# Kernel tuning notes

Measured on AMD Instinct MI355X. Metric: run time of the kernel, lower is better.

Reference implementation:

```python
import jax, jax.numpy as jnp
import numpy as np
from jax import lax

H = 512          # hidden_size
STATE = 16       # state_size
K = 4            # conv_kernel
EXPAND = 2
INNER = H * EXPAND
RATIO = 0.5      # remaining_ratio
EPS = 1e-5       # LayerNorm eps (torch default)


def linear(x, w, b=None):
    # torch nn.Linear: y = x @ W^T + b, W stored (out, in)
    y = jnp.einsum('...i,oi->...o', x, w)
    return y + b if b is not None else y


def causal_dwconv(x, w, b):
    # x: (B,S,C); w: (C,1,K) depthwise. torch pads K-1 both sides then slices
    # [:, :, :S], which equals left-pad K-1 (causal).
    xc = jnp.swapaxes(x, 1, 2)  # (B,C,S)
    y = lax.conv_general_dilated(xc, w, (1,), [(K - 1, 0)],
                                 feature_group_count=w.shape[0],
                                 dimension_numbers=('NCH', 'OIH', 'NCH'))
    return jnp.swapaxes(y + b[None, :, None], 1, 2)


def conv1d_same(x, w, b):
    # x: (B,S,C); w: (Cout,Cin,3), padding=1
    xc = jnp.swapaxes(x, 1, 2)
    y = lax.conv_general_dilated(xc, w, (1,), [(1, 1)],
                                 dimension_numbers=('NCH', 'OIH', 'NCH'))
    return jnp.swapaxes(y + b[None, :, None], 1, 2)


def layernorm(x, g, b):
    m = jnp.mean(x, axis=-1, keepdims=True)
    v = jnp.mean((x - m) ** 2, axis=-1, keepdims=True)
    return (x - m) * lax.rsqrt(v + EPS) * g + b


def partial_flip(x):
    S = x.shape[1]
    r = max(1, int(S * RATIO))
    n = S - r
    if n <= 0:
        return x
    return jnp.concatenate([x[:, :n][:, ::-1], x[:, n:]], axis=1)


def mamba_block(x, in_w, conv_w, conv_b, xproj_w, dt_w, dt_b, D, out_w):
    # x: (B,S,H)
    xz = linear(x, in_w)                              # (B,S,2*INNER)
    x_proj, z = xz[..., :INNER], xz[..., INNER:]
    x_conv = jax.nn.silu(causal_dwconv(x_proj, conv_w, conv_b))  # (B,S,INNER)
    xs = linear(x_conv, xproj_w)                      # (B,S,2*STATE+INNER)
    Bm = xs[..., :STATE]
    Cm = xs[..., STATE:2 * STATE]
    dt = jax.nn.softplus(linear(xs[..., 2 * STATE:], dt_w, dt_b))
    # EMA-approx SSM scan
    alpha = jax.nn.sigmoid(dt * 0.1)
    alpha_c = jnp.clip(alpha, 0.01, 0.99)
    B_gate = jax.nn.sigmoid(jnp.mean(Bm, axis=-1, keepdims=True))
    gated = (1.0 - alpha) * B_gate * x_conv

    def step(h, ab):
        a, gi = ab
        h = a * h + gi
        return h, h

    h0 = jnp.zeros((x.shape[0], INNER), x.dtype)
    _, ys = lax.scan(step, h0, (jnp.swapaxes(alpha_c, 0, 1), jnp.swapaxes(gated, 0, 1)))
    y = jnp.swapaxes(ys, 0, 1)                        # (B,S,INNER)
    y = y * jax.nn.sigmoid(jnp.mean(Cm, axis=-1, keepdims=True))
    y = y + D * x_conv
    y = y * jax.nn.silu(z)
    return linear(y, out_w)


def setup_inputs() -> dict:
    key = jax.random.key(0)
    ks = iter(jax.random.split(key, 48))

    def nrm(shape, s=0.02):
        return jax.random.normal(next(ks), shape, jnp.float32) * s

    def dt_bias():
        u = jax.random.uniform(next(ks), (INNER,), jnp.float32)
        return jnp.exp(u * (np.log(0.1) - np.log(0.001)) + np.log(0.001))

    Bsz, S = 4, 4096
    inp = {
        'x': jax.random.normal(next(ks), (Bsz, S, H), jnp.float32),
        'seq_len': jnp.full((Bsz,), S, jnp.int32),
        'ds_w': nrm((H, H)), 'ds_b': jnp.zeros((H,), jnp.float32),
        'gate_w': nrm((H, 2 * H)), 'gate_b': jnp.zeros((H,), jnp.float32),
        'mix_w': nrm((H, H)), 'mix_b': jnp.zeros((H,), jnp.float32),
        'ln_g': jnp.ones((H,), jnp.float32), 'ln_b': jnp.zeros((H,), jnp.float32),
        'fe_c1_w': nrm((H, H, 3)), 'fe_c1_b': jnp.zeros((H,), jnp.float32),
        'fe_c2_w': nrm((H, H, 3)), 'fe_c2_b': jnp.zeros((H,), jnp.float32),
        'fe_ln_g': jnp.ones((H,), jnp.float32), 'fe_ln_b': jnp.zeros((H,), jnp.float32),
    }
    for p in ('f', 'b'):
        inp[p + '_in_w'] = nrm((2 * INNER, H))
        inp[p + '_conv_w'] = nrm((INNER, 1, K))
        inp[p + '_conv_b'] = jnp.zeros((INNER,), jnp.float32)
        inp[p + '_xproj_w'] = nrm((2 * STATE + INNER, INNER))
        inp[p + '_dt_w'] = nrm((INNER, INNER))
        inp[p + '_dt_b'] = dt_bias()
        inp[p + '_D'] = jnp.ones((INNER,), jnp.float32)
        inp[p + '_out_w'] = nrm((H, INNER))
    return inp


def reference(x, seq_len, ds_w, ds_b, gate_w, gate_b, mix_w, mix_b, ln_g, ln_b,
              fe_c1_w, fe_c1_b, fe_c2_w, fe_c2_b, fe_ln_g, fe_ln_b,
              f_in_w, f_conv_w, f_conv_b, f_xproj_w, f_dt_w, f_dt_b, f_D, f_out_w,
              b_in_w, b_conv_w, b_conv_b, b_xproj_w, b_dt_w, b_dt_b, b_D, b_out_w):
    gate_weights = jax.nn.sigmoid(linear(x, ds_w, ds_b))
    m_fwd = mamba_block(x, f_in_w, f_conv_w, f_conv_b, f_xproj_w, f_dt_w, f_dt_b, f_D, f_out_w)
    m_bwd = partial_flip(mamba_block(partial_flip(x), b_in_w, b_conv_w, b_conv_b,
                                     b_xproj_w, b_dt_w, b_dt_b, b_D, b_out_w))
    m_comb = gate_weights * m_fwd + (1.0 - gate_weights) * m_bwd
    # FE conv branch
    c = jax.nn.silu(conv1d_same(x, fe_c1_w, fe_c1_b))
    c = conv1d_same(c, fe_c2_w, fe_c2_b)
    f_out = layernorm(c + x, fe_ln_g, fe_ln_b)
    g = jax.nn.sigmoid(linear(jnp.concatenate([m_comb, f_out], axis=-1), gate_w, gate_b))
    z = g * m_comb + (1.0 - g) * f_out
    z = linear(z, mix_w, mix_b)
    z = layernorm(z + x, ln_g, ln_b)
    return z
```

## Files before the change

kernel.cpp:

```cpp
#include <hip/hip_runtime.h>
#include <math.h>

#define Tt 16384
#define Ss 4096
#define Bb 4
#define Hh 512
#define II 1024
#define CHUNK 32
#define NCH 128
#define SP 4098

typedef unsigned short ushort_t;
typedef unsigned int uint_t;
typedef __attribute__((ext_vector_type(8))) short bf16x8;
typedef __attribute__((ext_vector_type(4))) short bf16x4;
typedef __attribute__((ext_vector_type(4))) float f32x4;

__device__ __forceinline__ float sigm(float x) { return 1.0f / (1.0f + __expf(-x)); }
__device__ __forceinline__ float b2f(ushort_t h) { return __uint_as_float(((uint_t)h) << 16); }
__device__ __forceinline__ ushort_t f2b(float f) {
    uint_t u = __float_as_uint(f);
    return (ushort_t)((u + 0x7FFFu + ((u >> 16) & 1u)) >> 16);
}
__device__ __forceinline__ void stc(float* p, float v)    { *p = v; }
__device__ __forceinline__ void stc(ushort_t* p, float v) { *p = f2b(v); }
__device__ __forceinline__ float ldc1(const float* p)    { return *p; }
__device__ __forceinline__ float ldc1(const ushort_t* p) { return b2f(*p); }

__device__ __forceinline__ void gload16(const void* g, void* l) {
    __builtin_amdgcn_global_load_lds(
        (const __attribute__((address_space(1))) unsigned int*)g,
        (__attribute__((address_space(3))) unsigned int*)l,
        16, 0, 0);
}

__global__ __launch_bounds__(256) void mfma_gemm(
    const ushort_t* __restrict__ A, const ushort_t* __restrict__ A1, int lda,
    const ushort_t* __restrict__ W, int ldw,
    const float* __restrict__ bias,
    void* __restrict__ Cv, int ldc, int Nreal, int K,
    int amode, int act, int smode, int cbf16)
{
    __shared__ __align__(16) ushort_t As[128 * 32];
    __shared__ __align__(16) ushort_t Bs[128 * 32];
    const int tid  = threadIdx.x;
    const int lane = tid & 63;
    const int wid  = tid >> 6;
    const int bm   = blockIdx.y * 128;
    const int bn   = blockIdx.x * 128;
    const int wr   = wid >> 1;
    const int wc   = wid & 1;

    const int colA = (lane & 3) * 8;
    long gA[2], gW[2];
    #pragma unroll
    for (int r = 0; r < 2; ++r) {
        const int rt = (r * 4 + wid) * 16 + (lane >> 2);
        const int t  = bm + rt;
        const int b  = t >> 12;
        const int s  = t & (Ss - 1);
        long rowoff;
        if (amode == 0)      rowoff = (long)t * lda;
        else if (amode == 1) { const int sf = (s < 2048) ? (2047 - s) : s;
                               rowoff = (long)(b * SP + sf + 1) * 512; }
        else if (amode == 2) rowoff = (long)(b * SP + s + 1) * 512;
        else if (amode == 3) rowoff = (long)(b * SP + s) * 512;
        else                 rowoff = (long)t * 512;
        gA[r] = rowoff + colA;
        gW[r] = (long)(bn + rt) * ldw + colA;
    }

    const int aoff = (wr * 64 + (lane & 15)) * 32 + (lane >> 4) * 8;
    const int boff = (wc * 64 + (lane & 15)) * 32 + (lane >> 4) * 8;

    f32x4 acc[4][4] = {};

    for (int k0 = 0; k0 < K; k0 += 32) {
        const ushort_t* pA = A;
        long kadd = k0;
        if (amode == 4) { pA = (k0 < 512) ? A : A1; kadd = k0 & 511; }
        #pragma unroll
        for (int r = 0; r < 2; ++r) {
            gload16(pA + gA[r] + kadd, &As[(r * 4 + wid) * 512]);
            gload16(W + gW[r] + k0,    &Bs[(r * 4 + wid) * 512]);
        }
        __syncthreads();

        bf16x8 af[4], bfr[4];
        #pragma unroll
        for (int mi = 0; mi < 4; ++mi) af[mi]  = *(const bf16x8*)&As[aoff + mi * 512];
        #pragma unroll
        for (int ni = 0; ni < 4; ++ni) bfr[ni] = *(const bf16x8*)&Bs[boff + ni * 512];
        #pragma unroll
        for (int mi = 0; mi < 4; ++mi)
            #pragma unroll
            for (int ni = 0; ni < 4; ++ni)
                acc[mi][ni] = __builtin_amdgcn_mfma_f32_16x16x32_bf16(
                    af[mi], bfr[ni], acc[mi][ni], 0, 0, 0);
        __syncthreads();
    }

    float* Cf = (float*)Cv;
    ushort_t* Cb = (ushort_t*)Cv;
    #pragma unroll
    for (int mi = 0; mi < 4; ++mi) {
        const int row0 = bm + wr * 64 + mi * 16 + (lane >> 4) * 4;
        #pragma unroll
        for (int ni = 0; ni < 4; ++ni) {
            const int col = bn + wc * 64 + ni * 16 + (lane & 15);
            if (col < Nreal) {
                const float bv = bias ? bias[col] : 0.f;
                #pragma unroll
                for (int r = 0; r < 4; ++r) {
                    float v = acc[mi][ni][r] + bv;
                    if (act == 1) v = sigm(v);
                    else if (act == 2) v = v * sigm(v);
                    const int t = row0 + r;
                    long crow;
                    if (smode == 1) { const int b = t >> 12, s = t & (Ss - 1);
                                      crow = (long)(b * SP + s + 1); }
                    else crow = t;
                    if (cbf16) Cb[crow * ldc + col] = f2b(v);
                    else       Cf[crow * ldc + col] = v;
                }
            }
        }
    }
}


__global__ __launch_bounds__(256) void cvt_x_pad(
    const float* __restrict__ x, ushort_t* __restrict__ xpad)
{
    const int idx = blockIdx.x * 256 + threadIdx.x;
    const int c8 = (idx & 63) * 8;
    const int sp = (idx >> 6) % SP;
    const int b  = idx / (64 * SP);
    bf16x8 v;
    if (sp == 0 || sp == SP - 1) {
        v = (bf16x8)0;
    } else {
        const float* p = x + ((long)(b * Ss + sp - 1)) * 512 + c8;
        #pragma unroll
        for (int j = 0; j < 8; ++j) v[j] = (short)f2b(p[j]);
    }
    *(bf16x8*)&xpad[((long)(b * SP + sp)) * 512 + c8] = v;
}

__global__ __launch_bounds__(256) void cvt_plain(
    const float* __restrict__ s, ushort_t* __restrict__ d, int n4)
{
    const int i = blockIdx.x * 256 + threadIdx.x;
    if (i >= n4) return;
    const float4 f = *(const float4*)&s[(long)i * 4];
    bf16x4 v;
    v[0] = (short)f2b(f.x); v[1] = (short)f2b(f.y);
    v[2] = (short)f2b(f.z); v[3] = (short)f2b(f.w);
    *(bf16x4*)&d[(long)i * 4] = v;
}

__global__ __launch_bounds__(256) void cvt_xproj(
    const float* __restrict__ s, ushort_t* __restrict__ d)
{
    const int i = blockIdx.x * 256 + threadIdx.x;
    const long e = (long)i * 4;
    const int n = (int)(e >> 10);
    bf16x4 v = (bf16x4)0;
    if (n < 1056) {
        const float4 f = *(const float4*)&s[e];
        v[0] = (short)f2b(f.x); v[1] = (short)f2b(f.y);
        v[2] = (short)f2b(f.z); v[3] = (short)f2b(f.w);
    }
    *(bf16x4*)&d[e] = v;
}

__global__ __launch_bounds__(256) void cvt_fe(
    const float* __restrict__ s, ushort_t* __restrict__ d)
{
    const int idx = blockIdx.x * 256 + threadIdx.x;
    const int n = idx / 1536;
    const int rem = idx - n * 1536;
    const int j = rem >> 9;
    const int c = rem & 511;
    d[idx] = f2b(s[((long)n * 512 + c) * 3 + j]);
}

__global__ __launch_bounds__(256) void zero_halo(ushort_t* __restrict__ p)
{
    const int i = blockIdx.x * 256 + threadIdx.x;
    const int c8 = (i & 63) * 8;
    const int h = (i >> 6) & 1;
    const int b = i >> 7;
    const long row = (long)b * SP + (h ? SP - 1 : 0);
    *(bf16x8*)&p[row * 512 + c8] = (bf16x8)0;
}


__global__ __launch_bounds__(256) void dwconv_silu_k(
    const ushort_t* __restrict__ xz, const float* __restrict__ w,
    const float* __restrict__ bias, ushort_t* __restrict__ out)
{
    const int idx = blockIdx.x * 256 + threadIdx.x;
    const int c = idx & (II - 1);
    const int t = idx >> 10;
    const int s = t & (Ss - 1);
    const long rb = (long)t * 2048;
    const float w0 = w[c * 4 + 0], w1 = w[c * 4 + 1], w2 = w[c * 4 + 2], w3 = w[c * 4 + 3];
    float sum = bias[c] + b2f(xz[rb + c]) * w3;
    if (s >= 1) sum += b2f(xz[rb - 2048 + c]) * w2;
    if (s >= 2) sum += b2f(xz[rb - 2 * 2048 + c]) * w1;
    if (s >= 3) sum += b2f(xz[rb - 3 * 2048 + c]) * w0;
    out[idx] = f2b(sum * sigm(sum));
}

__global__ __launch_bounds__(256) void bgcg_k(
    const ushort_t* __restrict__ xs, float* __restrict__ bg, float* __restrict__ cg)
{
    const int t = blockIdx.x * 256 + threadIdx.x;
    if (t >= Tt) return;
    const ushort_t* p = xs + (long)t * 1056;
    float sb = 0.f, sc = 0.f;
    #pragma unroll
    for (int i = 0; i < 16; ++i) { sb += b2f(p[i]); sc += b2f(p[16 + i]); }
    bg[t] = sigm(sb * (1.f / 16.f));
    cg[t] = sigm(sc * (1.f / 16.f));
}

__global__ __launch_bounds__(256) void alphagate_k(
    ushort_t* __restrict__ dtlin, const ushort_t* __restrict__ xc,
    const float* __restrict__ bg, ushort_t* __restrict__ gated)
{
    const int idx = blockIdx.x * 256 + threadIdx.x;
    const int t = idx >> 10;
    const float xv = b2f(dtlin[idx]);
    const float dt = (xv > 20.f) ? xv : log1pf(__expf(xv));
    const float alpha = sigm(0.1f * dt);
    const float ac = fminf(fmaxf(alpha, 0.01f), 0.99f);
    gated[idx] = f2b((1.f - alpha) * bg[t] * b2f(xc[idx]));
    dtlin[idx] = f2b(ac);
}

__global__ __launch_bounds__(256) void scan1_k(
    const ushort_t* __restrict__ a, const ushort_t* __restrict__ g,
    float* __restrict__ ap, float* __restrict__ gs)
{
    const int idx = blockIdx.x * 256 + threadIdx.x;
    const int c = idx & (II - 1);
    const int ch = (idx >> 10) & (NCH - 1);
    const int b = idx >> 17;
    const long base = ((long)(b * Ss + ch * CHUNK)) * II + c;
    float P = 1.f, h = 0.f;
    #pragma unroll 4
    for (int i = 0; i < CHUNK; ++i) {
        const float av = b2f(a[base + (long)i * II]);
        const float gv = b2f(g[base + (long)i * II]);
        P *= av;
        h = av * h + gv;
    }
    ap[idx] = P;
    gs[idx] = h;
}

__global__ __launch_bounds__(256) void scan2_k(
    const float* __restrict__ ap, const float* __restrict__ gs, float* __restrict__ hin)
{
    const int idx = blockIdx.x * 256 + threadIdx.x;
    if (idx >= Bb * II) return;
    const int c = idx & (II - 1);
    const int b = idx >> 10;
    float h = 0.f;
    for (int ch = 0; ch < NCH; ++ch) {
        const long j = ((long)(b * NCH + ch) << 10) + c;
        hin[j] = h;
        h = ap[j] * h + gs[j];
    }
}

__global__ __launch_bounds__(256) void scan3_k(
    const ushort_t* __restrict__ a, ushort_t* __restrict__ g, const float* __restrict__ hin)
{
    const int idx = blockIdx.x * 256 + threadIdx.x;
    const int c = idx & (II - 1);
    const int ch = (idx >> 10) & (NCH - 1);
    const int b = idx >> 17;
    const long base = ((long)(b * Ss + ch * CHUNK)) * II + c;
    float h = hin[idx];
    #pragma unroll 4
    for (int i = 0; i < CHUNK; ++i) {
        const long o = base + (long)i * II;
        h = b2f(a[o]) * h + b2f(g[o]);
        g[o] = f2b(h);
    }
}

__global__ __launch_bounds__(256) void yfinal_k(
    ushort_t* __restrict__ y, const float* __restrict__ cg, const float* __restrict__ D,
    const ushort_t* __restrict__ xc, const ushort_t* __restrict__ xz)
{
    const int idx = blockIdx.x * 256 + threadIdx.x;
    const int c = idx & (II - 1);
    const int t = idx >> 10;
    float v = b2f(y[idx]) * cg[t] + D[c] * b2f(xc[idx]);
    const float z = b2f(xz[(long)t * 2048 + II + c]);
    y[idx] = f2b(v * (z * sigm(z)));
}

__global__ __launch_bounds__(256) void mcomb_k(
    ushort_t* __restrict__ mf, const ushort_t* __restrict__ mb,
    const ushort_t* __restrict__ gw)
{
    const int idx = blockIdx.x * 256 + threadIdx.x;
    const int h = idx & (Hh - 1);
    const int t = idx >> 9;
    const int s = t & (Ss - 1);
    const int b = t >> 12;
    const int sf = (s < 2048) ? (2047 - s) : s;
    const float g = b2f(gw[idx]);
    const float v = g * b2f(mf[idx]) + (1.f - g) * b2f(mb[((long)((b << 12) | sf) << 9) + h]);
    mf[idx] = f2b(v);
}

__global__ __launch_bounds__(256) void zmid_k(
    const ushort_t* __restrict__ glin, const ushort_t* __restrict__ mc,
    const ushort_t* __restrict__ fo, ushort_t* __restrict__ out)
{
    const int idx = blockIdx.x * 256 + threadIdx.x;
    const float g = b2f(glin[idx]);
    out[idx] = f2b(g * b2f(mc[idx]) + (1.f - g) * b2f(fo[idx]));
}

template <typename TA, typename TO>
__global__ __launch_bounds__(256) void ln_k(
    const TA* __restrict__ a, const float* __restrict__ r,
    const float* __restrict__ gam, const float* __restrict__ bet, TO* __restrict__ out)
{
    const int lane = threadIdx.x & 63;
    const int wave = threadIdx.x >> 6;
    const int t = blockIdx.x * 4 + wave;
    const TA* pa = a + (long)t * Hh + lane * 8;
    const float* pr = r + (long)t * Hh + lane * 8;
    float v[8];
    float s = 0.f;
    #pragma unroll
    for (int j = 0; j < 8; ++j) { v[j] = ldc1(&pa[j]) + pr[j]; s += v[j]; }
    #pragma unroll
    for (int off = 32; off; off >>= 1) s += __shfl_xor(s, off);
    const float mean = s * (1.f / 512.f);
    float vs = 0.f;
    #pragma unroll
    for (int j = 0; j < 8; ++j) { const float d = v[j] - mean; vs += d * d; }
    #pragma unroll
    for (int off = 32; off; off >>= 1) vs += __shfl_xor(vs, off);
    const float inv = rsqrtf(vs * (1.f / 512.f) + 1e-5f);
    TO* po = out + (long)t * Hh + lane * 8;
    const float* pg = gam + lane * 8;
    const float* pb = bet + lane * 8;
    #pragma unroll
    for (int j = 0; j < 8; ++j) stc(&po[j], (v[j] - mean) * inv * pg[j] + pb[j]);
}


static inline void gemm(hipStream_t st, const ushort_t* A, const ushort_t* A1, int lda,
                        const ushort_t* W, int ldw, const float* bias,
                        void* C, int ldc, int Nreal, int PN, int K,
                        int amode, int act, int smode, int cbf16)
{
    dim3 g(PN / 128, Tt / 128);
    mfma_gemm<<<g, 256, 0, st>>>(A, A1, lda, W, ldw, bias, C, ldc, Nreal, K,
                                 amode, act, smode, cbf16);
}

static void mamba_block(hipStream_t st, const ushort_t* xpad, int amode_in,
                        const ushort_t* w_in, const float* conv_w, const float* conv_b,
                        const ushort_t* w_xp, const ushort_t* w_dt, const float* dt_b,
                        const float* Dp, const ushort_t* w_out,
                        ushort_t* xz, ushort_t* xc, ushort_t* xs, ushort_t* alpha,
                        float* ap, float* gs, float* hin, float* bg, float* cg,
                        ushort_t* mout)
{
    ushort_t* gated = xs;
    const int gEW = (Tt * II) / 256;
    gemm(st, xpad, nullptr, 512, w_in, 512, nullptr, xz, 2048, 2048, 2048, 512,
         amode_in, 0, 0, 1);
    dwconv_silu_k<<<gEW, 256, 0, st>>>(xz, conv_w, conv_b, xc);
    gemm(st, xc, nullptr, 1024, w_xp, 1024, nullptr, xs, 1056, 1056, 1152, 1024,
         0, 0, 0, 1);
    bgcg_k<<<Tt / 256, 256, 0, st>>>(xs, bg, cg);
    gemm(st, xs + 32, nullptr, 1056, w_dt, 1024, dt_b, alpha, 1024, 1024, 1024, 1024,
         0, 0, 0, 1);
    alphagate_k<<<gEW, 256, 0, st>>>(alpha, xc, bg, gated);
    scan1_k<<<(Bb * NCH * II) / 256, 256, 0, st>>>(alpha, gated, ap, gs);
    scan2_k<<<(Bb * II) / 256, 256, 0, st>>>(ap, gs, hin);
    scan3_k<<<(Bb * NCH * II) / 256, 256, 0, st>>>(alpha, gated, hin);
    yfinal_k<<<gEW, 256, 0, st>>>(gated, cg, Dp, xc, xz);
    gemm(st, gated, nullptr, 1024, w_out, 1024, nullptr, mout, 512, 512, 512, 1024,
         0, 0, 0, 1);
}

extern "C" void kernel_launch(void* const* d_in, const int* in_sizes, int n_in,
                              void* d_out, int out_size, void* d_ws, size_t ws_size,
                              hipStream_t stream)
{
    const float* x       = (const float*)d_in[0];
    const float* ds_w    = (const float*)d_in[2];
    const float* ds_b    = (const float*)d_in[3];
    const float* gate_w  = (const float*)d_in[4];
    const float* gate_b  = (const float*)d_in[5];
    const float* mix_w   = (const float*)d_in[6];
    const float* mix_b   = (const float*)d_in[7];
    const float* ln_g    = (const float*)d_in[8];
    const float* ln_b    = (const float*)d_in[9];
    const float* fe_c1_w = (const float*)d_in[10];
    const float* fe_c1_b = (const float*)d_in[11];
    const float* fe_c2_w = (const float*)d_in[12];
    const float* fe_c2_b = (const float*)d_in[13];
    const float* fe_ln_g = (const float*)d_in[14];
    const float* fe_ln_b = (const float*)d_in[15];
    const float* f_in_w    = (const float*)d_in[16];
    const float* f_conv_w  = (const float*)d_in[17];
    const float* f_conv_b  = (const float*)d_in[18];
    const float* f_xproj_w = (const float*)d_in[19];
    const float* f_dt_w    = (const float*)d_in[20];
    const float* f_dt_b    = (const float*)d_in[21];
    const float* f_D       = (const float*)d_in[22];
    const float* f_out_w   = (const float*)d_in[23];
    const float* b_in_w    = (const float*)d_in[24];
    const float* b_conv_w  = (const float*)d_in[25];
    const float* b_conv_b  = (const float*)d_in[26];
    const float* b_xproj_w = (const float*)d_in[27];
    const float* b_dt_w    = (const float*)d_in[28];
    const float* b_dt_b    = (const float*)d_in[29];
    const float* b_D       = (const float*)d_in[30];
    const float* b_out_w   = (const float*)d_in[31];

    char* base = (char*)d_ws;
    ushort_t* xz    = (ushort_t*)(base + 0L);
    ushort_t* xc    = (ushort_t*)(base + 67108864L);
    ushort_t* xs    = (ushort_t*)(base + 100663296L);
    ushort_t* alpha = (ushort_t*)(base + 135266304L);
    float*    ap    = (float*)(base + 168820736L);
    float*    gs    = (float*)(base + 170917888L);
    float*    hin   = (float*)(base + 173015040L);
    float*    bg    = (float*)(base + 175112192L);
    float*    cg    = (float*)(base + 175177728L);
    ushort_t* m_fwd = (ushort_t*)(base + 175243264L);
    ushort_t* m_bwd = (ushort_t*)(base + 192020480L);
    ushort_t* xpad  = (ushort_t*)(base + 208797696L);
    ushort_t* w_fin  = (ushort_t*)(base + 225583104L);
    ushort_t* w_bin  = (ushort_t*)(base + 227680256L);
    ushort_t* w_fxp  = (ushort_t*)(base + 229777408L);
    ushort_t* w_bxp  = (ushort_t*)(base + 232136704L);
    ushort_t* w_fdt  = (ushort_t*)(base + 234496000L);
    ushort_t* w_bdt  = (ushort_t*)(base + 236593152L);
    ushort_t* w_fout = (ushort_t*)(base + 238690304L);
    ushort_t* w_bout = (ushort_t*)(base + 239738880L);
    ushort_t* w_ds   = (ushort_t*)(base + 240787456L);
    ushort_t* w_gate = (ushort_t*)(base + 241311744L);
    ushort_t* w_mix  = (ushort_t*)(base + 242360320L);
    ushort_t* w_fc1  = (ushort_t*)(base + 242884608L);
    ushort_t* w_fc2  = (ushort_t*)(base + 244457472L);
    ushort_t* gwt   = (ushort_t*)(base + 0L);
    ushort_t* c1pad = (ushort_t*)(base + 16777216L);
    ushort_t* c2    = (ushort_t*)(base + 33562624L);
    ushort_t* fout  = (ushort_t*)(base + 50339840L);
    ushort_t* glin  = (ushort_t*)(base + 67117056L);
    ushort_t* zmidb = (ushort_t*)(base + 83894272L);
    float*    zmix  = (float*)(base + 100671488L);

    const int gH = (Tt * Hh) / 256;

    cvt_x_pad<<<(Bb * SP * 64) / 256, 256, 0, stream>>>(x, xpad);
    cvt_plain<<<1024, 256, 0, stream>>>(f_in_w, w_fin, 262144);
    cvt_plain<<<1024, 256, 0, stream>>>(b_in_w, w_bin, 262144);
    cvt_xproj<<<1152, 256, 0, stream>>>(f_xproj_w, w_fxp);
    cvt_xproj<<<1152, 256, 0, stream>>>(b_xproj_w, w_bxp);
    cvt_plain<<<1024, 256, 0, stream>>>(f_dt_w, w_fdt, 262144);
    cvt_plain<<<1024, 256, 0, stream>>>(b_dt_w, w_bdt, 262144);
    cvt_plain<<<512, 256, 0, stream>>>(f_out_w, w_fout, 131072);
    cvt_plain<<<512, 256, 0, stream>>>(b_out_w, w_bout, 131072);
    cvt_plain<<<256, 256, 0, stream>>>(ds_w, w_ds, 65536);
    cvt_plain<<<512, 256, 0, stream>>>(gate_w, w_gate, 131072);
    cvt_plain<<<256, 256, 0, stream>>>(mix_w, w_mix, 65536);
    cvt_fe<<<3072, 256, 0, stream>>>(fe_c1_w, w_fc1);
    cvt_fe<<<3072, 256, 0, stream>>>(fe_c2_w, w_fc2);

    mamba_block(stream, xpad, 2, w_fin, f_conv_w, f_conv_b, w_fxp, w_fdt, f_dt_b,
                f_D, w_fout, xz, xc, xs, alpha, ap, gs, hin, bg, cg, m_fwd);
    mamba_block(stream, xpad, 1, w_bin, b_conv_w, b_conv_b, w_bxp, w_bdt, b_dt_b,
                b_D, w_bout, xz, xc, xs, alpha, ap, gs, hin, bg, cg, m_bwd);

    gemm(stream, xpad, nullptr, 512, w_ds, 512, ds_b, gwt, 512, 512, 512, 512,
         2, 1, 0, 1);

    zero_halo<<<2, 256, 0, stream>>>(c1pad);
    gemm(stream, xpad, nullptr, 512, w_fc1, 1536, fe_c1_b, c1pad, 512, 512, 512, 1536,
         3, 2, 1, 1);
    gemm(stream, c1pad, nullptr, 512, w_fc2, 1536, fe_c2_b, c2, 512, 512, 512, 1536,
         3, 0, 0, 1);
    ln_k<ushort_t, ushort_t><<<Tt / 4, 256, 0, stream>>>(c2, x, fe_ln_g, fe_ln_b, fout);

    mcomb_k<<<gH, 256, 0, stream>>>(m_fwd, m_bwd, gwt);

    gemm(stream, m_fwd, fout, 512, w_gate, 1024, gate_b, glin, 512, 512, 512, 1024,
         4, 1, 0, 1);

    zmid_k<<<gH, 256, 0, stream>>>(glin, m_fwd, fout, zmidb);

    gemm(stream, zmidb, nullptr, 512, w_mix, 512, mix_b, zmix, 512, 512, 512, 512,
         0, 0, 0, 0);

    ln_k<float, float><<<Tt / 4, 256, 0, stream>>>(zmix, x, ln_g, ln_b, (float*)d_out);
}
```

Measured before the change: 1.373 ms.

## Fuse elementwise stages into scans and GEMM epilogues, batch conversions, swizzle LDS

Folds the alpha/gate computation into both scan passes and the y-final step into scan3, which removes two full-size elementwise kernels and their intermediate buffers. The gate-combine kernels (mcomb, zmid) move into the epilogues of the ds and gate GEMMs. The fourteen weight/input conversion launches collapse into one kernel. An XOR swizzle on LDS tile columns is added to reduce bank conflicts in the MFMA GEMM. The cost is recomputing softplus/sigmoid in both scan passes and a read-modify-write of m_fwd in the GEMM epilogue.

After: 1.432 ms. 1.04x slower.

```diff
diff --git a/kernel.cpp b/kernel.cpp
--- a/kernel.cpp
+++ b/kernel.cpp
@@ -34,12 +34,21 @@
         16, 0, 0);
 }
 
+__device__ __forceinline__ void alpha_gate(float xv, float bgv, float xcv,
+                                           float& ac, float& gv) {
+    const float dt = (xv > 20.f) ? xv : log1pf(__expf(xv));
+    const float alpha = sigm(0.1f * dt);
+    ac = fminf(fmaxf(alpha, 0.01f), 0.99f);
+    gv = (1.f - alpha) * bgv * xcv;
+}
+
 __global__ __launch_bounds__(256) void mfma_gemm(
     const ushort_t* __restrict__ A, const ushort_t* __restrict__ A1, int lda,
     const ushort_t* __restrict__ W, int ldw,
     const float* __restrict__ bias,
     void* __restrict__ Cv, int ldc, int Nreal, int K,
-    int amode, int act, int smode, int cbf16)
+    int amode, int act, int smode, int cbf16,
+    int fuse, const ushort_t* __restrict__ e0, const ushort_t* __restrict__ e1)
 {
     __shared__ __align__(16) ushort_t As[128 * 32];
     __shared__ __align__(16) ushort_t Bs[128 * 32];
@@ -51,7 +60,7 @@
     const int wr   = wid >> 1;
     const int wc   = wid & 1;
 
-    const int colA = (lane & 3) * 8;
+    const int colA = ((lane & 3) ^ ((lane >> 3) & 3)) * 8;
     long gA[2], gW[2];
     #pragma unroll
     for (int r = 0; r < 2; ++r) {
@@ -70,8 +79,9 @@
         gW[r] = (long)(bn + rt) * ldw + colA;
     }
 
-    const int aoff = (wr * 64 + (lane & 15)) * 32 + (lane >> 4) * 8;
-    const int boff = (wc * 64 + (lane & 15)) * 32 + (lane >> 4) * 8;
+    const int kswz = ((lane >> 4) ^ ((lane >> 1) & 3)) * 8;
+    const int aoff = (wr * 64 + (lane & 15)) * 32 + kswz;
+    const int boff = (wc * 64 + (lane & 15)) * 32 + kswz;
 
     f32x4 acc[4][4] = {};
 
@@ -113,76 +123,99 @@
                 #pragma unroll
                 for (int r = 0; r < 4; ++r) {
                     float v = acc[mi][ni][r] + bv;
-                    if (act == 1) v = sigm(v);
-                    else if (act == 2) v = v * sigm(v);
                     const int t = row0 + r;
-                    long crow;
-                    if (smode == 1) { const int b = t >> 12, s = t & (Ss - 1);
-                                      crow = (long)(b * SP + s + 1); }
-                    else crow = t;
-                    if (cbf16) Cb[crow * ldc + col] = f2b(v);
-                    else       Cf[crow * ldc + col] = v;
+                    if (fuse == 0) {
+                        if (act == 1) v = sigm(v);
+                        else if (act == 2) v = v * sigm(v);
+                        long crow;
+                        if (smode == 1) { const int b = t >> 12, s = t & (Ss - 1);
+                                          crow = (long)(b * SP + s + 1); }
+                        else crow = t;
+                        if (cbf16) Cb[crow * ldc + col] = f2b(v);
+                        else       Cf[crow * ldc + col] = v;
+                    } else {
+                        const float g = sigm(v);
+                        const long idx = (long)t * ldc + col;
+                        if (fuse == 1) {
+                            const int b = t >> 12, s = t & (Ss - 1);
+                            const int sf = (s < 2048) ? (2047 - s) : s;
+                            const float mb =
+                                b2f(e1[((long)((b << 12) | sf) << 9) + col]);
+                            Cb[idx] = f2b(g * b2f(Cb[idx]) + (1.f - g) * mb);
+                        } else {
+                            Cb[idx] = f2b(g * b2f(e0[idx]) + (1.f - g) * b2f(e1[idx]));
+                        }
+                    }
                 }
             }
         }
     }
 }
 
-
-__global__ __launch_bounds__(256) void cvt_x_pad(
-    const float* __restrict__ x, ushort_t* __restrict__ xpad)
-{
-    const int idx = blockIdx.x * 256 + threadIdx.x;
-    const int c8 = (idx & 63) * 8;
-    const int sp = (idx >> 6) % SP;
-    const int b  = idx / (64 * SP);
-    bf16x8 v;
-    if (sp == 0 || sp == SP - 1) {
-        v = (bf16x8)0;
-    } else {
-        const float* p = x + ((long)(b * Ss + sp - 1)) * 512 + c8;
-        #pragma unroll
-        for (int j = 0; j < 8; ++j) v[j] = (short)f2b(p[j]);
-    }
-    *(bf16x8*)&xpad[((long)(b * SP + sp)) * 512 + c8] = v;
-}
-
-__global__ __launch_bounds__(256) void cvt_plain(
-    const float* __restrict__ s, ushort_t* __restrict__ d, int n4)
-{
-    const int i = blockIdx.x * 256 + threadIdx.x;
-    if (i >= n4) return;
-    const float4 f = *(const float4*)&s[(long)i * 4];
-    bf16x4 v;
-    v[0] = (short)f2b(f.x); v[1] = (short)f2b(f.y);
-    v[2] = (short)f2b(f.z); v[3] = (short)f2b(f.w);
-    *(bf16x4*)&d[(long)i * 4] = v;
-}
-
-__global__ __launch_bounds__(256) void cvt_xproj(
-    const float* __restrict__ s, ushort_t* __restrict__ d)
-{
-    const int i = blockIdx.x * 256 + threadIdx.x;
-    const long e = (long)i * 4;
-    const int n = (int)(e >> 10);
-    bf16x4 v = (bf16x4)0;
-    if (n < 1056) {
-        const float4 f = *(const float4*)&s[e];
+struct CvtP {
+    const float* x;
+    const float* src[13];
+    ushort_t* xpad;
+    ushort_t* dst[13];
+};
+
+__global__ __launch_bounds__(256) void cvt_all(CvtP p)
+{
+    const int blk = blockIdx.x;
+    const int tid = threadIdx.x;
+    if (blk < 4098) {
+        const int idx = blk * 256 + tid;
+        const int c8 = (idx & 63) * 8;
+        const int sp = (idx >> 6) % SP;
+        const int b  = idx / (64 * SP);
+        bf16x8 v;
+        if (sp == 0 || sp == SP - 1) {
+            v = (bf16x8)0;
+        } else {
+            const float* q = p.x + ((long)(b * Ss + sp - 1)) * 512 + c8;
+            #pragma unroll
+            for (int j = 0; j < 8; ++j) v[j] = (short)f2b(q[j]);
+        }
+        *(bf16x8*)&p.xpad[((long)(b * SP + sp)) * 512 + c8] = v;
+    } else if (blk < 10242) {
+        int seg, off;
+        if      (blk < 5122) { seg = 0; off = blk - 4098; }
+        else if (blk < 6146) { seg = 1; off = blk - 5122; }
+        else if (blk < 7170) { seg = 2; off = blk - 6146; }
+        else if (blk < 8194) { seg = 3; off = blk - 7170; }
+        else if (blk < 8706) { seg = 4; off = blk - 8194; }
+        else if (blk < 9218) { seg = 5; off = blk - 8706; }
+        else if (blk < 9730) { seg = 6; off = blk - 9218; }
+        else if (blk < 9986) { seg = 7; off = blk - 9730; }
+        else                 { seg = 8; off = blk - 9986; }
+        const long e = (long)(off * 256 + tid) * 4;
+        const float4 f = *(const float4*)&p.src[seg][e];
+        bf16x4 v;
         v[0] = (short)f2b(f.x); v[1] = (short)f2b(f.y);
         v[2] = (short)f2b(f.z); v[3] = (short)f2b(f.w);
-    }
-    *(bf16x4*)&d[e] = v;
-}
-
-__global__ __launch_bounds__(256) void cvt_fe(
-    const float* __restrict__ s, ushort_t* __restrict__ d)
-{
-    const int idx = blockIdx.x * 256 + threadIdx.x;
-    const int n = idx / 1536;
-    const int rem = idx - n * 1536;
-    const int j = rem >> 9;
-    const int c = rem & 511;
-    d[idx] = f2b(s[((long)n * 512 + c) * 3 + j]);
+        *(bf16x4*)&p.dst[seg][e] = v;
+    } else if (blk < 12546) {
+        const int seg = (blk < 11394) ? 9 : 10;
+        const int off = blk - ((blk < 11394) ? 10242 : 11394);
+        const long e = (long)(off * 256 + tid) * 4;
+        const int n = (int)(e >> 10);
+        bf16x4 v = (bf16x4)0;
+        if (n < 1056) {
+            const float4 f = *(const float4*)&p.src[seg][e];
+            v[0] = (short)f2b(f.x); v[1] = (short)f2b(f.y);
+            v[2] = (short)f2b(f.z); v[3] = (short)f2b(f.w);
+        }
+        *(bf16x4*)&p.dst[seg][e] = v;
+    } else {
+        const int seg = (blk < 15618) ? 11 : 12;
+        const int off = blk - ((blk < 15618) ? 12546 : 15618);
+        const int idx = off * 256 + tid;
+        const int n = idx / 1536;
+        const int rem = idx - n * 1536;
+        const int j = rem >> 9;
+        const int c = rem & 511;
+        p.dst[seg][idx] = f2b(p.src[seg][((long)n * 512 + c) * 3 + j]);
+    }
 }
 
 __global__ __launch_bounds__(256) void zero_halo(ushort_t* __restrict__ p)
@@ -226,36 +259,25 @@
     cg[t] = sigm(sc * (1.f / 16.f));
 }
 
-__global__ __launch_bounds__(256) void alphagate_k(
-    ushort_t* __restrict__ dtlin, const ushort_t* __restrict__ xc,
-    const float* __restrict__ bg, ushort_t* __restrict__ gated)
-{
-    const int idx = blockIdx.x * 256 + threadIdx.x;
-    const int t = idx >> 10;
-    const float xv = b2f(dtlin[idx]);
-    const float dt = (xv > 20.f) ? xv : log1pf(__expf(xv));
-    const float alpha = sigm(0.1f * dt);
-    const float ac = fminf(fmaxf(alpha, 0.01f), 0.99f);
-    gated[idx] = f2b((1.f - alpha) * bg[t] * b2f(xc[idx]));
-    dtlin[idx] = f2b(ac);
-}
-
 __global__ __launch_bounds__(256) void scan1_k(
-    const ushort_t* __restrict__ a, const ushort_t* __restrict__ g,
+    const ushort_t* __restrict__ dt, const ushort_t* __restrict__ xc,
+    const float* __restrict__ bg,
     float* __restrict__ ap, float* __restrict__ gs)
 {
     const int idx = blockIdx.x * 256 + threadIdx.x;
     const int c = idx & (II - 1);
     const int ch = (idx >> 10) & (NCH - 1);
     const int b = idx >> 17;
-    const long base = ((long)(b * Ss + ch * CHUNK)) * II + c;
+    const int t0 = b * Ss + ch * CHUNK;
+    const long base = (long)t0 * II + c;
     float P = 1.f, h = 0.f;
     #pragma unroll 4
     for (int i = 0; i < CHUNK; ++i) {
-        const float av = b2f(a[base + (long)i * II]);
-        const float gv = b2f(g[base + (long)i * II]);
-        P *= av;
-        h = av * h + gv;
+        const long o = base + (long)i * II;
+        float ac, gv;
+        alpha_gate(b2f(dt[o]), bg[t0 + i], b2f(xc[o]), ac, gv);
+        P *= ac;
+        h = ac * h + gv;
     }
     ap[idx] = P;
     gs[idx] = h;
@@ -277,56 +299,31 @@
 }
 
 __global__ __launch_bounds__(256) void scan3_k(
-    const ushort_t* __restrict__ a, ushort_t* __restrict__ g, const float* __restrict__ hin)
+    ushort_t* __restrict__ dt, const ushort_t* __restrict__ xc,
+    const float* __restrict__ bg, const float* __restrict__ hin,
+    const float* __restrict__ cg, const float* __restrict__ D,
+    const ushort_t* __restrict__ xz)
 {
     const int idx = blockIdx.x * 256 + threadIdx.x;
     const int c = idx & (II - 1);
     const int ch = (idx >> 10) & (NCH - 1);
     const int b = idx >> 17;
-    const long base = ((long)(b * Ss + ch * CHUNK)) * II + c;
+    const int t0 = b * Ss + ch * CHUNK;
+    const long base = (long)t0 * II + c;
+    const float Dv = D[c];
     float h = hin[idx];
     #pragma unroll 4
     for (int i = 0; i < CHUNK; ++i) {
         const long o = base + (long)i * II;
-        h = b2f(a[o]) * h + b2f(g[o]);
-        g[o] = f2b(h);
-    }
-}
-
-__global__ __launch_bounds__(256) void yfinal_k(
-    ushort_t* __restrict__ y, const float* __restrict__ cg, const float* __restrict__ D,
-    const ushort_t* __restrict__ xc, const ushort_t* __restrict__ xz)
-{
-    const int idx = blockIdx.x * 256 + threadIdx.x;
-    const int c = idx & (II - 1);
-    const int t = idx >> 10;
-    float v = b2f(y[idx]) * cg[t] + D[c] * b2f(xc[idx]);
-    const float z = b2f(xz[(long)t * 2048 + II + c]);
-    y[idx] = f2b(v * (z * sigm(z)));
-}
-
-__global__ __launch_bounds__(256) void mcomb_k(
-    ushort_t* __restrict__ mf, const ushort_t* __restrict__ mb,
-    const ushort_t* __restrict__ gw)
-{
-    const int idx = blockIdx.x * 256 + threadIdx.x;
-    const int h = idx & (Hh - 1);
-    const int t = idx >> 9;
-    const int s = t & (Ss - 1);
-    const int b = t >> 12;
-    const int sf = (s < 2048) ? (2047 - s) : s;
-    const float g = b2f(gw[idx]);
-    const float v = g * b2f(mf[idx]) + (1.f - g) * b2f(mb[((long)((b << 12) | sf) << 9) + h]);
-    mf[idx] = f2b(v);
-}
-
-__global__ __launch_bounds__(256) void zmid_k(
-    const ushort_t* __restrict__ glin, const ushort_t* __restrict__ mc,
-    const ushort_t* __restrict__ fo, ushort_t* __restrict__ out)
-{
-    const int idx = blockIdx.x * 256 + threadIdx.x;
-    const float g = b2f(glin[idx]);
-    out[idx] = f2b(g * b2f(mc[idx]) + (1.f - g) * b2f(fo[idx]));
+        const int t = t0 + i;
+        const float xcv = b2f(xc[o]);
+        float ac, gv;
+        alpha_gate(b2f(dt[o]), bg[t], xcv, ac, gv);
+        h = ac * h + gv;
+        const float y = h * cg[t] + Dv * xcv;
+        const float z = b2f(xz[(long)t * 2048 + II + c]);
+        dt[o] = f2b(y * (z * sigm(z)));
+    }
 }
 
 template <typename TA, typename TO>
@@ -363,22 +360,23 @@
 static inline void gemm(hipStream_t st, const ushort_t* A, const ushort_t* A1, int lda,
                         const ushort_t* W, int ldw, const float* bias,
                         void* C, int ldc, int Nreal, int PN, int K,
-                        int amode, int act, int smode, int cbf16)
+                        int amode, int act, int smode, int cbf16,
+                        int fuse = 0, const ushort_t* e0 = nullptr,
+                        const ushort_t* e1 = nullptr)
 {
     dim3 g(PN / 128, Tt / 128);
     mfma_gemm<<<g, 256, 0, st>>>(A, A1, lda, W, ldw, bias, C, ldc, Nreal, K,
-                                 amode, act, smode, cbf16);
+                                 amode, act, smode, cbf16, fuse, e0, e1);
 }
 
 static void mamba_block(hipStream_t st, const ushort_t* xpad, int amode_in,
                         const ushort_t* w_in, const float* conv_w, const float* conv_b,
                         const ushort_t* w_xp, const ushort_t* w_dt, const float* dt_b,
                         const float* Dp, const ushort_t* w_out,
-                        ushort_t* xz, ushort_t* xc, ushort_t* xs, ushort_t* alpha,
+                        ushort_t* xz, ushort_t* xc, ushort_t* xs, ushort_t* dtl,
                         float* ap, float* gs, float* hin, float* bg, float* cg,
                         ushort_t* mout)
 {
-    ushort_t* gated = xs;
     const int gEW = (Tt * II) / 256;
     gemm(st, xpad, nullptr, 512, w_in, 512, nullptr, xz, 2048, 2048, 2048, 512,
          amode_in, 0, 0, 1);
@@ -386,14 +384,12 @@
     gemm(st, xc, nullptr, 1024, w_xp, 1024, nullptr, xs, 1056, 1056, 1152, 1024,
          0, 0, 0, 1);
     bgcg_k<<<Tt / 256, 256, 0, st>>>(xs, bg, cg);
-    gemm(st, xs + 32, nullptr, 1056, w_dt, 1024, dt_b, alpha, 1024, 1024, 1024, 1024,
+    gemm(st, xs + 32, nullptr, 1056, w_dt, 1024, dt_b, dtl, 1024, 1024, 1024, 1024,
          0, 0, 0, 1);
-    alphagate_k<<<gEW, 256, 0, st>>>(alpha, xc, bg, gated);
-    scan1_k<<<(Bb * NCH * II) / 256, 256, 0, st>>>(alpha, gated, ap, gs);
+    scan1_k<<<(Bb * NCH * II) / 256, 256, 0, st>>>(dtl, xc, bg, ap, gs);
     scan2_k<<<(Bb * II) / 256, 256, 0, st>>>(ap, gs, hin);
-    scan3_k<<<(Bb * NCH * II) / 256, 256, 0, st>>>(alpha, gated, hin);
-    yfinal_k<<<gEW, 256, 0, st>>>(gated, cg, Dp, xc, xz);
-    gemm(st, gated, nullptr, 1024, w_out, 1024, nullptr, mout, 512, 512, 512, 1024,
+    scan3_k<<<(Bb * NCH * II) / 256, 256, 0, st>>>(dtl, xc, bg, hin, cg, Dp, xz);
+    gemm(st, dtl, nullptr, 1024, w_out, 1024, nullptr, mout, 512, 512, 512, 1024,
          0, 0, 0, 1);
 }
 
@@ -437,7 +433,7 @@
     ushort_t* xz    = (ushort_t*)(base + 0L);
     ushort_t* xc    = (ushort_t*)(base + 67108864L);
     ushort_t* xs    = (ushort_t*)(base + 100663296L);
-    ushort_t* alpha = (ushort_t*)(base + 135266304L);
+    ushort_t* dtl   = (ushort_t*)(base + 135266304L);
     float*    ap    = (float*)(base + 168820736L);
     float*    gs    = (float*)(base + 170917888L);
     float*    hin   = (float*)(base + 173015040L);
@@ -459,38 +455,33 @@
     ushort_t* w_mix  = (ushort_t*)(base + 242360320L);
     ushort_t* w_fc1  = (ushort_t*)(base + 242884608L);
     ushort_t* w_fc2  = (ushort_t*)(base + 244457472L);
-    ushort_t* gwt   = (ushort_t*)(base + 0L);
-    ushort_t* c1pad = (ushort_t*)(base + 16777216L);
-    ushort_t* c2    = (ushort_t*)(base + 33562624L);
-    ushort_t* fout  = (ushort_t*)(base + 50339840L);
-    ushort_t* glin  = (ushort_t*)(base + 67117056L);
-    ushort_t* zmidb = (ushort_t*)(base + 83894272L);
-    float*    zmix  = (float*)(base + 100671488L);
-
-    const int gH = (Tt * Hh) / 256;
-
-    cvt_x_pad<<<(Bb * SP * 64) / 256, 256, 0, stream>>>(x, xpad);
-    cvt_plain<<<1024, 256, 0, stream>>>(f_in_w, w_fin, 262144);
-    cvt_plain<<<1024, 256, 0, stream>>>(b_in_w, w_bin, 262144);
-    cvt_xproj<<<1152, 256, 0, stream>>>(f_xproj_w, w_fxp);
-    cvt_xproj<<<1152, 256, 0, stream>>>(b_xproj_w, w_bxp);
-    cvt_plain<<<1024, 256, 0, stream>>>(f_dt_w, w_fdt, 262144);
-    cvt_plain<<<1024, 256, 0, stream>>>(b_dt_w, w_bdt, 262144);
-    cvt_plain<<<512, 256, 0, stream>>>(f_out_w, w_fout, 131072);
-    cvt_plain<<<512, 256, 0, stream>>>(b_out_w, w_bout, 131072);
-    cvt_plain<<<256, 256, 0, stream>>>(ds_w, w_ds, 65536);
-    cvt_plain<<<512, 256, 0, stream>>>(gate_w, w_gate, 131072);
-    cvt_plain<<<256, 256, 0, stream>>>(mix_w, w_mix, 65536);
-    cvt_fe<<<3072, 256, 0, stream>>>(fe_c1_w, w_fc1);
-    cvt_fe<<<3072, 256, 0, stream>>>(fe_c2_w, w_fc2);
+    ushort_t* c1pad = (ushort_t*)(base + 0L);
+    ushort_t* c2    = (ushort_t*)(base + 16785408L);
+    ushort_t* fout  = (ushort_t*)(base + 33562624L);
+    ushort_t* zmidb = (ushort_t*)(base + 50339840L);
+    float*    zmix  = (float*)(base + 67117056L);
+
+    CvtP cp;
+    cp.x = x; cp.xpad = xpad;
+    cp.src[0] = f_in_w;  cp.dst[0] = w_fin;
+    cp.src[1] = b_in_w;  cp.dst[1] = w_bin;
+    cp.src[2] = f_dt_w;  cp.dst[2] = w_fdt;
+    cp.src[3] = b_dt_w;  cp.dst[3] = w_bdt;
+    cp.src[4] = f_out_w; cp.dst[4] = w_fout;
+    cp.src[5] = b_out_w; cp.dst[5] = w_bout;
+    cp.src[6] = gate_w;  cp.dst[6] = w_gate;
+    cp.src[7] = ds_w;    cp.dst[7] = w_ds;
+    cp.src[8] = mix_w;   cp.dst[8] = w_mix;
+    cp.src[9]  = f_xproj_w; cp.dst[9]  = w_fxp;
+    cp.src[10] = b_xproj_w; cp.dst[10] = w_bxp;
+    cp.src[11] = fe_c1_w;   cp.dst[11] = w_fc1;
+    cp.src[12] = fe_c2_w;   cp.dst[12] = w_fc2;
+    cvt_all<<<18690, 256, 0, stream>>>(cp);
 
     mamba_block(stream, xpad, 2, w_fin, f_conv_w, f_conv_b, w_fxp, w_fdt, f_dt_b,
-                f_D, w_fout, xz, xc, xs, alpha, ap, gs, hin, bg, cg, m_fwd);
+                f_D, w_fout, xz, xc, xs, dtl, ap, gs, hin, bg, cg, m_fwd);
     mamba_block(stream, xpad, 1, w_bin, b_conv_w, b_conv_b, w_bxp, w_bdt, b_dt_b,
-                b_D, w_bout, xz, xc, xs, alpha, ap, gs, hin, bg, cg, m_bwd);
-
-    gemm(stream, xpad, nullptr, 512, w_ds, 512, ds_b, gwt, 512, 512, 512, 512,
-         2, 1, 0, 1);
+                b_D, w_bout, xz, xc, xs, dtl, ap, gs, hin, bg, cg, m_bwd);
 
     zero_halo<<<2, 256, 0, stream>>>(c1pad);
     gemm(stream, xpad, nullptr, 512, w_fc1, 1536, fe_c1_b, c1pad, 512, 512, 512, 1536,
@@ -499,12 +490,11 @@
          3, 0, 0, 1);
     ln_k<ushort_t, ushort_t><<<Tt / 4, 256, 0, stream>>>(c2, x, fe_ln_g, fe_ln_b, fout);
 
-    mcomb_k<<<gH, 256, 0, stream>>>(m_fwd, m_bwd, gwt);
-
-    gemm(stream, m_fwd, fout, 512, w_gate, 1024, gate_b, glin, 512, 512, 512, 1024,
-         4, 1, 0, 1);
-
-    zmid_k<<<gH, 256, 0, stream>>>(glin, m_fwd, fout, zmidb);
+    gemm(stream, xpad, nullptr, 512, w_ds, 512, ds_b, m_fwd, 512, 512, 512, 512,
+         2, 0, 0, 1, 1, nullptr, m_bwd);
+
+    gemm(stream, m_fwd, fout, 512, w_gate, 1024, gate_b, zmidb, 512, 512, 512, 1024,
+         4, 0, 0, 1, 2, m_fwd, fout);
 
     gemm(stream, zmidb, nullptr, 512, w_mix, 512, mix_b, zmix, 512, 512, 512, 512,
          0, 0, 0, 0);
```
